# Optimization experiments

Hardware: AMD Instinct MI355X
Metric: run time of the kernel (lower is better)

Reference implementation:

```python
import jax, jax.numpy as jnp
import numpy as np

BS, C, T = 8, 4096, 512          # batch, channels/tokens, flattened spatial (= q_dim)
H, HD = 8, 64                     # n_heads, head_dim = output_dim // n_heads
OUT_DIM = 512
SCALE = float(np.sqrt(OUT_DIM))   # module uses sqrt(output_dim), not sqrt(head_dim)


def setup_inputs() -> dict:
    key = jax.random.key(0)
    ks = jax.random.split(key, 7)
    init = 0.02
    return {
        "q": jax.random.normal(ks[0], (BS, C, T), jnp.float32),
        "k": jax.random.normal(ks[1], (BS, C, T), jnp.float32),
        "v": jax.random.normal(ks[2], (BS, C, T), jnp.float32),
        # per-head Linear weights, torch layout (out, in) stacked over heads
        "Wq": jax.random.normal(ks[3], (H, HD, T), jnp.float32) * init,
        "Wk": jax.random.normal(ks[4], (H, HD, T), jnp.float32) * init,
        "Wv": jax.random.normal(ks[5], (H, HD, T), jnp.float32) * init,
        "Wo": jax.random.normal(ks[6], (OUT_DIM, H * HD), jnp.float32) * init,
    }


def reference(q, k, v, Wq, Wk, Wv, Wo):
    bs, c, t = q.shape
    # batched per-head projections: (b, C, T) x (H, HD, T) -> (b, H, C, HD)
    qh = jnp.einsum("bct,hdt->bhcd", q, Wq)
    kh = jnp.einsum("bct,hdt->bhcd", k, Wk)
    vh = jnp.einsum("bct,hdt->bhcd", v, Wv)
    # attention contracts over the channel axis c (faithful to 'bct,bcs->bts')
    scores = jnp.einsum("bhcd,bhce->bhde", qh, kh) / SCALE  # (b, H, HD, HD)
    w = jax.nn.softmax(scores, axis=-1)
    # 'bts,bcs->bct' per head -> (b, H, C, HD)
    attn = jnp.einsum("bhde,bhce->bhcd", w, vh)
    # concat heads along last dim: (b, C, H*HD)
    cat = attn.transpose(0, 2, 1, 3).reshape(bs, c, H * HD)
    out = cat @ Wo.T  # (b, C, OUT_DIM); dropout p=0 -> identity
    return out.reshape(bs, -1, t)  # view(bs, -1, *spatial)
```

## Files before the change

### kernel.cpp

```cpp
#include <hip/hip_runtime.h>

#define BS    8
#define CDIM  4096
#define TDIM  512
#define NH    8
#define HD    64
#define NDIM  512
#define INV_SCALE 0.044194173824159216f

typedef __bf16 bf16x8 __attribute__((ext_vector_type(8)));
typedef float  f32x4  __attribute__((ext_vector_type(4)));

static __device__ __forceinline__ unsigned short f2b(float f) {
    union { float f; unsigned int i; } x; x.f = f;
    unsigned int r = x.i + 0x7FFFu + ((x.i >> 16) & 1u);
    return (unsigned short)(r >> 16);
}

static __device__ __forceinline__ void gl2lds16(const unsigned short* g,
                                                unsigned short* l) {
    __builtin_amdgcn_global_load_lds(
        (const __attribute__((address_space(1))) void*)g,
        (__attribute__((address_space(3))) void*)l, 16, 0, 0);
}

__global__ __launch_bounds__(256) void transpose_qk_kernel(
    const float* __restrict__ q, const float* __restrict__ k,
    unsigned short* __restrict__ qT, unsigned short* __restrict__ kT)
{
    __shared__ unsigned short Ls[64 * 65];

    const int z = blockIdx.z;
    const int b = z & 7;
    const float* src = (z >> 3) ? k : q;
    unsigned short* dst = (z >> 3) ? kT : qT;

    const int c0 = blockIdx.x * 64;
    const int t0 = blockIdx.y * 64;
    const int tid = threadIdx.x;

    {
        const int r = tid >> 2, seg = (tid & 3) * 16;
        const float* p = src + ((size_t)b * CDIM + c0 + r) * TDIM + t0 + seg;
        float4 f0 = *(const float4*)p, f1 = *(const float4*)(p + 4);
        float4 f2 = *(const float4*)(p + 8), f3 = *(const float4*)(p + 12);
        float ff[16] = {f0.x, f0.y, f0.z, f0.w, f1.x, f1.y, f1.z, f1.w,
                        f2.x, f2.y, f2.z, f2.w, f3.x, f3.y, f3.z, f3.w};
#pragma unroll
        for (int j = 0; j < 16; j++) Ls[(seg + j) * 65 + r] = f2b(ff[j]);
    }
    __syncthreads();
    {
        const int tp = tid >> 2, cs = (tid & 3) * 16;
        alignas(16) unsigned short u[16];
#pragma unroll
        for (int j = 0; j < 16; j++) u[j] = Ls[tp * 65 + cs + j];
        unsigned short* o = dst + ((size_t)b * TDIM + t0 + tp) * CDIM + c0 + cs;
        *(float4*)o = *(const float4*)u;
        *(float4*)(o + 8) = *(const float4*)(u + 8);
    }
}

__global__ __launch_bounds__(256) void cvt_kernel(
    const float* __restrict__ in, unsigned short* __restrict__ out, int n8)
{
    int i = blockIdx.x * 256 + threadIdx.x;
    if (i >= n8) return;
    float4 f0 = ((const float4*)in)[i * 2], f1 = ((const float4*)in)[i * 2 + 1];
    alignas(16) unsigned short t[8] = {f2b(f0.x), f2b(f0.y), f2b(f0.z), f2b(f0.w),
                                       f2b(f1.x), f2b(f1.y), f2b(f1.z), f2b(f1.w)};
    ((float4*)out)[i] = *(const float4*)t;
}

__global__ __launch_bounds__(256) void gemm128_kernel(
    const unsigned short* __restrict__ A, size_t sAb,
    const unsigned short* __restrict__ B, size_t sBb,
    void* __restrict__ Cv, int c_f32, int writeT, int ldc, size_t sCb,
    int ldk, int K, int zshift, int zmask, size_t sCsplit)
{
    __shared__ unsigned short As[5][128 * 32];
    __shared__ unsigned short Bs[5][128 * 32];

    const int tid  = threadIdx.x;
    const int wave = tid >> 6, lane = tid & 63;
    const int quad = lane >> 4, l16 = lane & 15;
    const int wm = wave >> 1, wn = wave & 1;
    const int m0 = blockIdx.x * 128, n0 = blockIdx.y * 128;
    const int z = blockIdx.z;
    const int b = z >> zshift, ks = z & zmask;
    const int kbase = ks * K;

    const unsigned short* Ab = A + (size_t)b * sAb;
    const unsigned short* Bb = B + (size_t)b * sBb;

    f32x4 acc[4][4];
#pragma unroll
    for (int i = 0; i < 4; i++)
#pragma unroll
        for (int j = 0; j < 4; j++) acc[i][j] = (f32x4){0.f, 0.f, 0.f, 0.f};

    const int ldr  = lane >> 2;
    const int fr_w = (ldr & 3) ^ ((ldr >> 2) & 1);
    const int gcol = ((lane & 3) ^ fr_w) * 8;
    const int fr_r = (l16 & 3) ^ ((l16 >> 2) & 1);
    const int qsw  = (quad ^ fr_r) * 8;

    const int nt = K / 32;

    auto stage = [&](int t) {
        const int kk = kbase + t * 32;
        unsigned short* as = &As[t % 5][0];
        unsigned short* bs = &Bs[t % 5][0];
#pragma unroll
        for (int i = 0; i < 2; i++) {
            const int panel = wave * 2 + i;
            gl2lds16(&Ab[(size_t)(m0 + panel * 16 + ldr) * ldk + kk + gcol],
                     &as[panel * 512]);
            gl2lds16(&Bb[(size_t)(n0 + panel * 16 + ldr) * ldk + kk + gcol],
                     &bs[panel * 512]);
        }
    };

    stage(0);
    if (nt > 1) stage(1);
    if (nt > 2) stage(2);

    for (int t = 0; t < nt; ++t) {
        if (t + 3 < nt) stage(t + 3);
        const int ahead = nt - 1 - t;
        if (ahead >= 3)      asm volatile("s_waitcnt vmcnt(12)" ::: "memory");
        else if (ahead == 2) asm volatile("s_waitcnt vmcnt(8)"  ::: "memory");
        else if (ahead == 1) asm volatile("s_waitcnt vmcnt(4)"  ::: "memory");
        else                 asm volatile("s_waitcnt vmcnt(0)"  ::: "memory");
        __builtin_amdgcn_s_barrier();
        asm volatile("" ::: "memory");

        const unsigned short* as = &As[t % 5][0];
        const unsigned short* bs = &Bs[t % 5][0];
        bf16x8 af[4], bf[4];
#pragma unroll
        for (int i = 0; i < 4; i++) {
            af[i] = *(const bf16x8*)&as[(wm * 64 + i * 16 + l16) * 32 + qsw];
            bf[i] = *(const bf16x8*)&bs[(wn * 64 + i * 16 + l16) * 32 + qsw];
        }
#pragma unroll
        for (int mb = 0; mb < 4; mb++)
#pragma unroll
            for (int nb = 0; nb < 4; nb++)
                acc[mb][nb] = __builtin_amdgcn_mfma_f32_16x16x32_bf16(
                    af[mb], bf[nb], acc[mb][nb], 0, 0, 0);
    }

    const size_t offC = (size_t)b * sCb + (size_t)ks * sCsplit;
#pragma unroll
    for (int mb = 0; mb < 4; mb++)
#pragma unroll
        for (int nb = 0; nb < 4; nb++)
#pragma unroll
            for (int r = 0; r < 4; r++) {
                int row = m0 + wm * 64 + mb * 16 + quad * 4 + r;
                int col = n0 + wn * 64 + nb * 16 + l16;
                size_t idx = offC + (writeT ? (size_t)col * ldc + row
                                            : (size_t)row * ldc + col);
                if (c_f32) ((float*)Cv)[idx] = acc[mb][nb][r];
                else ((unsigned short*)Cv)[idx] = f2b(acc[mb][nb][r]);
            }
}

__global__ __launch_bounds__(256) void reduceG_kernel(
    const float* __restrict__ P, unsigned short* __restrict__ G)
{
    const int i = blockIdx.x * 256 + threadIdx.x;
    const float4* p = (const float4*)P + (size_t)i * 2;
    const size_t st = 2097152 / 4;
    float4 a0 = p[0], a1 = p[1];
#pragma unroll
    for (int s = 1; s < 4; s++) {
        float4 b0 = p[(size_t)s * st], b1 = p[(size_t)s * st + 1];
        a0.x += b0.x; a0.y += b0.y; a0.z += b0.z; a0.w += b0.w;
        a1.x += b1.x; a1.y += b1.y; a1.z += b1.z; a1.w += b1.w;
    }
    alignas(16) unsigned short t[8] = {f2b(a0.x), f2b(a0.y), f2b(a0.z), f2b(a0.w),
                                       f2b(a1.x), f2b(a1.y), f2b(a1.z), f2b(a1.w)};
    ((float4*)G)[i] = *(const float4*)t;
}

__global__ __launch_bounds__(256) void gemm64_kernel(
    const void* __restrict__ Av, int a_f32, size_t sAb, size_t sAh,
    const unsigned short* __restrict__ B, size_t sBb, size_t sBh,
    void* __restrict__ Cv, int c_f32, int writeT, int ldc, size_t sCb, size_t sCh,
    int K, int hshift, int hmask)
{
    __shared__ unsigned short As[64][40];
    __shared__ unsigned short Bs[64][40];

    const int tid  = threadIdx.x;
    const int wave = tid >> 6, lane = tid & 63;
    const int quad = lane >> 4, l16 = lane & 15;
    const int m0 = blockIdx.x * 64, n0 = blockIdx.y * 64;
    const int bz = blockIdx.z;
    const int b = bz >> hshift, h = bz & hmask;

    f32x4 acc[4];
#pragma unroll
    for (int i = 0; i < 4; i++) acc[i] = (f32x4){0.f, 0.f, 0.f, 0.f};

    const int ldrow = tid >> 2, ldseg = (tid & 3) * 8;
    const size_t offA = (size_t)b * sAb + (size_t)h * sAh;
    const size_t offB = (size_t)b * sBb + (size_t)h * sBh;

    for (int k0 = 0; k0 < K; k0 += 32) {
        __syncthreads();
        if (a_f32) {
            const float* p = (const float*)Av + offA + (size_t)(m0 + ldrow) * K + k0 + ldseg;
            float4 lo = *(const float4*)p, hi = *(const float4*)(p + 4);
            alignas(16) unsigned short t8[8] = {
                f2b(lo.x), f2b(lo.y), f2b(lo.z), f2b(lo.w),
                f2b(hi.x), f2b(hi.y), f2b(hi.z), f2b(hi.w)};
            *(float4*)&As[ldrow][ldseg] = *(const float4*)t8;
        } else {
            const unsigned short* p = (const unsigned short*)Av + offA +
                                      (size_t)(m0 + ldrow) * K + k0 + ldseg;
            *(float4*)&As[ldrow][ldseg] = *(const float4*)p;
        }
        {
            const unsigned short* p = B + offB + (size_t)(n0 + ldrow) * K + k0 + ldseg;
            *(float4*)&Bs[ldrow][ldseg] = *(const float4*)p;
        }
        __syncthreads();

        bf16x8 a = *(const bf16x8*)&As[wave * 16 + l16][quad * 8];
#pragma unroll
        for (int nb = 0; nb < 4; nb++) {
            bf16x8 bb = *(const bf16x8*)&Bs[nb * 16 + l16][quad * 8];
            acc[nb] = __builtin_amdgcn_mfma_f32_16x16x32_bf16(a, bb, acc[nb], 0, 0, 0);
        }
    }

    const size_t offC = (size_t)b * sCb + (size_t)h * sCh;
#pragma unroll
    for (int nb = 0; nb < 4; nb++)
#pragma unroll
        for (int r = 0; r < 4; r++) {
            int row = m0 + wave * 16 + quad * 4 + r;
            int col = n0 + nb * 16 + l16;
            size_t idx = offC + (writeT ? (size_t)col * ldc + row
                                        : (size_t)row * ldc + col);
            if (c_f32) ((float*)Cv)[idx] = acc[nb][r];
            else ((unsigned short*)Cv)[idx] = f2b(acc[nb][r]);
        }
}

__global__ __launch_bounds__(256) void transpose_wv_kernel(
    const float* __restrict__ Wv, unsigned short* __restrict__ WvT)
{
    int i = blockIdx.x * 256 + threadIdx.x;
    int h = i >> 15, r = i & 32767;
    int t = r >> 6, e = i & 63;
    WvT[i] = f2b(Wv[(size_t)h * 32768 + (size_t)e * 512 + t]);
}

__global__ __launch_bounds__(64) void softmax_kernel(
    const float* __restrict__ S, unsigned short* __restrict__ w)
{
    const int bh = blockIdx.x;
    const int d  = threadIdx.x;
    const float* s = S + (size_t)bh * (HD * HD) + d * HD;
    float v[64];
    float m = -1e30f;
#pragma unroll
    for (int e = 0; e < 64; e++) { v[e] = s[e] * INV_SCALE; m = fmaxf(m, v[e]); }
    float sum = 0.f;
#pragma unroll
    for (int e = 0; e < 64; e++) { v[e] = __expf(v[e] - m); sum += v[e]; }
    float rinv = 1.0f / sum;
    unsigned short* o = w + (size_t)bh * (HD * HD) + d * HD;
#pragma unroll
    for (int e = 0; e < 64; e++) o[e] = f2b(v[e] * rinv);
}

extern "C" void kernel_launch(void* const* d_in, const int* in_sizes, int n_in,
                              void* d_out, int out_size, void* d_ws, size_t ws_size,
                              hipStream_t stream)
{
    const float* q  = (const float*)d_in[0];
    const float* k  = (const float*)d_in[1];
    const float* v  = (const float*)d_in[2];
    const float* Wq = (const float*)d_in[3];
    const float* Wk = (const float*)d_in[4];
    const float* Wv = (const float*)d_in[5];
    const float* Wo = (const float*)d_in[6];

    unsigned short* qT   = (unsigned short*)d_ws;
    unsigned short* kT   = qT + 16777216;
    unsigned short* G    = kT + 16777216;
    unsigned short* tmpT = G + 2097152;
    unsigned short* WkB  = tmpT + 2097152;
    unsigned short* WoB  = WkB + 262144;
    unsigned short* WvT  = WoB + 262144;
    unsigned short* w    = WvT + 262144;
    unsigned short* WveT = w + 262144;
    unsigned short* W2   = WveT + 2097152;
    float*          S    = (float*)(W2 + 2097152);
    float*          P1   = (float*)tmpT;
    unsigned short* vB   = qT;
    float*          PK   = (float*)kT;

    transpose_qk_kernel<<<dim3(64, 8, 16), 256, 0, stream>>>(q, k, qT, kT);

    gemm128_kernel<<<dim3(4, 4, BS * 4), 256, 0, stream>>>(
        qT, 2097152, kT, 2097152,
        P1, 1, 0, 512, 262144, 4096, 1024, 2, 3, 2097152);

    cvt_kernel<<<8192, 256, 0, stream>>>(v, vB, 2097152);

    reduceG_kernel<<<1024, 256, 0, stream>>>(P1, G);

    cvt_kernel<<<128, 256, 0, stream>>>(Wk, WkB, 32768);
    cvt_kernel<<<128, 256, 0, stream>>>(Wo, WoB, 32768);
    transpose_wv_kernel<<<1024, 256, 0, stream>>>(Wv, WvT);

    gemm128_kernel<<<dim3(4, 4, BS * 4), 256, 0, stream>>>(
        G, 262144, WkB, 0,
        PK, 1, 1, 512, 262144, 512, 128, 2, 3, 2097152);
    reduceG_kernel<<<1024, 256, 0, stream>>>(PK, tmpT);

    gemm64_kernel<<<dim3(1, 1, 64), 256, 0, stream>>>(
        Wq, 1, 0, 32768, tmpT, 262144, 32768,
        S, 1, 0, 64, 32768, 4096, 512, 3, 7);

    softmax_kernel<<<64, 64, 0, stream>>>(S, w);

    gemm64_kernel<<<dim3(1, 8, 64), 256, 0, stream>>>(
        w, 0, 32768, 4096, WvT, 0, 32768,
        WveT, 0, 1, 512, 262144, 64, 64, 3, 7);

    gemm128_kernel<<<dim3(4, 4, BS * 4), 256, 0, stream>>>(
        WoB, 0, WveT, 262144,
        PK, 1, 0, 512, 262144, 512, 128, 2, 3, 2097152);
    reduceG_kernel<<<1024, 256, 0, stream>>>(PK, W2);

    gemm128_kernel<<<dim3(32, 4, BS), 256, 0, stream>>>(
        vB, 2097152, W2, 262144,
        d_out, 1, 0, 512, 2097152, 512, 512, 0, 0, 0);
}
```

Baseline: 385.1 us.

## Pack bf16 pairs in transpose LDS and drop split-K for small GEMMs

The q/k transpose kernel now packs two bf16 values from adjacent channels into one 32-bit LDS word. Each thread loads two rows, which halves the LDS store count and allows wider reads on the way out. The two 512x512 per-batch GEMMs (G·Wk and Wo·Wve) were split-K gemm128 launches, each followed by a reduceG kernel. They are replaced by single gemm64 launches over a 64x64 tile grid with no K split. This removes the fp32 partial-sum traffic and two kernel launches, at the cost of a longer K loop per block.

```diff
diff --git a/kernel.cpp b/kernel.cpp
--- a/kernel.cpp
+++ b/kernel.cpp
@@ -28,7 +28,7 @@
     const float* __restrict__ q, const float* __restrict__ k,
     unsigned short* __restrict__ qT, unsigned short* __restrict__ kT)
 {
-    __shared__ unsigned short Ls[64 * 65];
+    __shared__ unsigned int Ls[64 * 33];
 
     const int z = blockIdx.z;
     const int b = z & 7;
@@ -40,24 +40,27 @@
     const int tid = threadIdx.x;
 
     {
-        const int r = tid >> 2, seg = (tid & 3) * 16;
-        const float* p = src + ((size_t)b * CDIM + c0 + r) * TDIM + t0 + seg;
-        float4 f0 = *(const float4*)p, f1 = *(const float4*)(p + 4);
-        float4 f2 = *(const float4*)(p + 8), f3 = *(const float4*)(p + 12);
-        float ff[16] = {f0.x, f0.y, f0.z, f0.w, f1.x, f1.y, f1.z, f1.w,
-                        f2.x, f2.y, f2.z, f2.w, f3.x, f3.y, f3.z, f3.w};
-#pragma unroll
-        for (int j = 0; j < 16; j++) Ls[(seg + j) * 65 + r] = f2b(ff[j]);
+        const int cp = tid >> 3, seg = (tid & 7) * 8;
+        const float* p0 = src + ((size_t)b * CDIM + c0 + 2 * cp) * TDIM + t0 + seg;
+        const float* p1 = p0 + TDIM;
+        float4 a0 = *(const float4*)p0, a1 = *(const float4*)(p0 + 4);
+        float4 b0 = *(const float4*)p1, b1 = *(const float4*)(p1 + 4);
+        float r0[8] = {a0.x, a0.y, a0.z, a0.w, a1.x, a1.y, a1.z, a1.w};
+        float r1[8] = {b0.x, b0.y, b0.z, b0.w, b1.x, b1.y, b1.z, b1.w};
+#pragma unroll
+        for (int j = 0; j < 8; j++)
+            Ls[(seg + j) * 33 + cp] =
+                (unsigned int)f2b(r0[j]) | ((unsigned int)f2b(r1[j]) << 16);
     }
     __syncthreads();
     {
-        const int tp = tid >> 2, cs = (tid & 3) * 16;
-        alignas(16) unsigned short u[16];
-#pragma unroll
-        for (int j = 0; j < 16; j++) u[j] = Ls[tp * 65 + cs + j];
-        unsigned short* o = dst + ((size_t)b * TDIM + t0 + tp) * CDIM + c0 + cs;
-        *(float4*)o = *(const float4*)u;
-        *(float4*)(o + 8) = *(const float4*)(u + 8);
+        const int tp = tid >> 2, cs = (tid & 3) * 8;
+        alignas(16) unsigned int u[8];
+#pragma unroll
+        for (int j = 0; j < 8; j++) u[j] = Ls[tp * 33 + cs + j];
+        unsigned short* o = dst + ((size_t)b * TDIM + t0 + tp) * CDIM + c0 + cs * 2;
+        *(uint4*)o       = *(const uint4*)&u[0];
+        *(uint4*)(o + 8) = *(const uint4*)&u[4];
     }
 }
 
@@ -304,7 +307,6 @@
     float*          S    = (float*)(W2 + 2097152);
     float*          P1   = (float*)tmpT;
     unsigned short* vB   = qT;
-    float*          PK   = (float*)kT;
 
     transpose_qk_kernel<<<dim3(64, 8, 16), 256, 0, stream>>>(q, k, qT, kT);
 
@@ -320,10 +322,9 @@
     cvt_kernel<<<128, 256, 0, stream>>>(Wo, WoB, 32768);
     transpose_wv_kernel<<<1024, 256, 0, stream>>>(Wv, WvT);
 
-    gemm128_kernel<<<dim3(4, 4, BS * 4), 256, 0, stream>>>(
-        G, 262144, WkB, 0,
-        PK, 1, 1, 512, 262144, 512, 128, 2, 3, 2097152);
-    reduceG_kernel<<<1024, 256, 0, stream>>>(PK, tmpT);
+    gemm64_kernel<<<dim3(8, 8, 8), 256, 0, stream>>>(
+        G, 0, 262144, 0, WkB, 0, 0,
+        tmpT, 0, 1, 512, 262144, 0, 512, 0, 0);
 
     gemm64_kernel<<<dim3(1, 1, 64), 256, 0, stream>>>(
         Wq, 1, 0, 32768, tmpT, 262144, 32768,
@@ -335,10 +336,9 @@
         w, 0, 32768, 4096, WvT, 0, 32768,
         WveT, 0, 1, 512, 262144, 64, 64, 3, 7);
 
-    gemm128_kernel<<<dim3(4, 4, BS * 4), 256, 0, stream>>>(
-        WoB, 0, WveT, 262144,
-        PK, 1, 0, 512, 262144, 512, 128, 2, 3, 2097152);
-    reduceG_kernel<<<1024, 256, 0, stream>>>(PK, W2);
+    gemm64_kernel<<<dim3(8, 8, 8), 256, 0, stream>>>(
+        WoB, 0, 0, 0, WveT, 262144, 0,
+        W2, 0, 0, 512, 262144, 0, 512, 0, 0);
 
     gemm128_kernel<<<dim3(32, 4, BS), 256, 0, stream>>>(
         vB, 2097152, W2, 262144,
```

Result: faster. 367.0 us (-4.7%).
